# Kernel optimization log

Measured on AMD Instinct MI355X. Metric: run time of the kernel, lower is better.

## Reference

```python
import jax, jax.numpy as jnp
import numpy as np

NEG = -1e30  # finite stand-in for -inf to keep gradients NaN-free


def setup_inputs() -> dict:
    key = jax.random.key(0)
    k1, k2, k3 = jax.random.split(key, 3)
    T, B, V, L = 1600, 48, 1000, 128
    # acoustic model output: already log-softmax normalized, layout [T, B, V]
    logits = jax.random.normal(k1, (T, B, V), dtype=jnp.float32)
    log_probs = jax.nn.log_softmax(logits, axis=-1)
    # flat concatenated targets (nonzero labels; 0 is blank), uniform length L per utt
    targets = jax.random.randint(k2, (B * L,), 1, V, dtype=jnp.int32)
    input_lengths = jax.random.randint(k3, (B,), 3 * T // 4, T + 1, dtype=jnp.int32)
    target_lengths = jnp.full((B,), L, dtype=jnp.int32)
    return {
        "log_probs": log_probs,
        "targets": targets,
        "input_lengths": input_lengths,
        "target_lengths": target_lengths,
    }


def _ctc_neg_log_likelihood(log_probs, targets, input_lengths, target_lengths):
    """Exact log-semiring CTC forward (total score over all alignments),
    equivalent to k2.intersect_dense(ctc_topo o linear_fsa, dense) +
    get_tot_scores(log_semiring=True). Returns -sum_b log p(y_b | x_b).
    log_probs: [T, B, V]; targets: flat [B*L]; lengths: [B].
    """
    T, B, V = log_probs.shape
    L = targets.shape[0] // B
    tg = targets.reshape(B, L)
    S = 2 * L + 1  # blank-interleaved extended label sequence

    ext = jnp.zeros((B, S), dtype=jnp.int32).at[:, 1::2].set(tg)  # [B, S]
    # skip transition s-2 -> s allowed iff label[s] != blank and != label[s-2]
    allow_skip = jnp.concatenate(
        [jnp.zeros((B, 2), dtype=bool),
         (ext[:, 2:] != 0) & (ext[:, 2:] != ext[:, :-2])],
        axis=1,
    )

    def emit(lp_t):  # [B, V] -> [B, S]
        return jnp.take_along_axis(lp_t, ext, axis=1)

    e0 = emit(log_probs[0])
    alpha0 = jnp.full((B, S), NEG, dtype=log_probs.dtype)
    alpha0 = alpha0.at[:, 0].set(e0[:, 0]).at[:, 1].set(e0[:, 1])

    def step(alpha, xs):
        lp_t, t = xs
        prev1 = jnp.pad(alpha[:, :-1], ((0, 0), (1, 0)), constant_values=NEG)
        prev2 = jnp.pad(alpha[:, :-2], ((0, 0), (2, 0)), constant_values=NEG)
        a = jnp.logaddexp(alpha, prev1)
        a = jnp.where(allow_skip, jnp.logaddexp(a, prev2), a)
        new = a + emit(lp_t)
        # freeze alpha once past each utterance's input length
        alpha = jnp.where((t < input_lengths)[:, None], new, alpha)
        return alpha, None

    alpha, _ = jax.lax.scan(step, alpha0, (log_probs[1:], jnp.arange(1, T)))

    # all target_lengths are L, so the final states are S-1 (last blank) and S-2
    tot_scores = jnp.logaddexp(alpha[:, S - 1], alpha[:, S - 2])  # [B]
    return -jnp.sum(tot_scores)


def reference(log_probs, targets, input_lengths, target_lengths):
    return _ctc_neg_log_likelihood(log_probs, targets, input_lengths, target_lengths)
```

## Files before the change

kernel.cpp:

```cpp
#include <hip/hip_runtime.h>
#include <math.h>

#define TT 1600
#define BB 48
#define VV 1000
#define LL 128
#define EMS 132
#define EMTOT (TT*EMS)
#define TILE 60
#define TILEF (TILE*EMS)
#define NTILES ((TT + TILE - 1)/TILE)

__global__ __launch_bounds__(256) void ctc_gather_kernel(
    const float* __restrict__ lp,
    const int* __restrict__ targets,
    float* __restrict__ em)
{
  __shared__ float rowbuf[4][1024];
  const int wv   = threadIdx.x >> 6;
  const int lane = threadIdx.x & 63;
  const int wid  = blockIdx.x * 4 + wv;
  const int t    = wid / BB;
  const int b    = wid - t * BB;

  const float* __restrict__ row = lp + (size_t)wid * VV;
  float* rb = rowbuf[wv];
#pragma unroll
  for (int i = 0; i < 4; i++) {
    int idx = lane + 64 * i;
    if (idx < 250) ((float4*)rb)[idx] = ((const float4*)row)[idx];
  }
  __syncthreads();

  const int* __restrict__ tg = targets + b * LL;
  float* __restrict__ erow = em + (size_t)b * EMTOT + (size_t)t * EMS;
#pragma unroll
  for (int ii = 0; ii < 3; ii++) {
    int k = lane + 64 * ii;
    if (k < 129) {
      int lab = (k == 0) ? 0 : tg[k - 1];
      int pos = (k == 0) ? 0 : (k + 1);
      erow[pos] = __expf(rb[lab]);
    }
  }
}

__global__ __launch_bounds__(128) void ctc_dp_kernel(
    const float* __restrict__ em,
    const int* __restrict__ targets,
    const int* __restrict__ input_lengths,
    float* __restrict__ out)
{
  __shared__ float sbuf[2][TILEF];
  const int b    = blockIdx.x;
  const int lane = threadIdx.x & 63;
  const int wv   = threadIdx.x >> 6;
  const int NS   = input_lengths[b] - 1;
  const float* __restrict__ base = em + (size_t)b * EMTOT;

  float skip1 = 0.f, skip3 = 0.f, m63 = 0.f;
  if (wv == 0) {
    const int* __restrict__ tg = targets + b * LL;
    const int c0  = tg[2 * lane];
    const int c1  = tg[2 * lane + 1];
    const int cm1 = (lane > 0) ? tg[2 * lane - 1] : c0;
    skip1 = (lane > 0 && c0 != cm1) ? 1.0f : 0.0f;
    skip3 = (c1 != c0) ? 1.0f : 0.0f;
    m63   = (lane == 63) ? 1.0f : 0.0f;
  }

  float a0 = 0.f, a1 = 0.f, a2 = 0.f, a3 = 0.f, a4 = 0.f;
  int esum = 0;
  float  pb_r[4];
  float2 ev_r[4];

  if (wv == 1) {
    const float4* src = (const float4*)base;
    float4* dst = (float4*)sbuf[0];
    for (int j = 0; j < 31; j++) {
      int idx = j * 64 + lane;
      if (idx < (TILEF >> 2)) dst[idx] = src[idx];
    }
  }
  __syncthreads();

#define STEP(PB, EV) do {                                            \
    float am1 = __shfl_up(a3, 1);                                    \
    am1 = (lane == 0) ? 0.f : am1;                                   \
    float s0 = a0 + am1;                                             \
    float s1 = fmaf(skip1, am1, a0 + a1);                            \
    float s2 = a1 + a2;                                              \
    float s3 = fmaf(skip3, a1, a2 + a3);                             \
    float s4 = fmaf(a3, m63, a4);                                    \
    a0 = s0 * (PB); a1 = s1 * (EV).x; a2 = s2 * (PB);                \
    a3 = s3 * (EV).y; a4 = s4 * (PB);                                \
  } while (0)

#define RESCALE() do {                                               \
    float mx = fmaxf(fmaxf(fmaxf(a0, a1), fmaxf(a2, a3)), a4);       \
    mx = fmaxf(mx, __shfl_xor(mx, 32));                              \
    mx = fmaxf(mx, __shfl_xor(mx, 16));                              \
    mx = fmaxf(mx, __shfl_xor(mx, 8));                               \
    mx = fmaxf(mx, __shfl_xor(mx, 4));                               \
    mx = fmaxf(mx, __shfl_xor(mx, 2));                               \
    mx = fmaxf(mx, __shfl_xor(mx, 1));                               \
    int eb = (int)((__float_as_uint(mx) >> 23) & 0xFF);              \
    int se = 157 - eb;                       \
    se = se < -126 ? -126 : (se > 127 ? 127 : se);                   \
    float sc = __uint_as_float((unsigned)(se + 127) << 23);          \
    a0 *= sc; a1 *= sc; a2 *= sc; a3 *= sc; a4 *= sc;                \
    esum -= se;                                                      \
  } while (0)

  for (int k = 0; k < NTILES; k++) {
    if (wv == 1) {
      int kn = k + 1;
      if (kn < NTILES) {
        const float4* src = (const float4*)(base + (size_t)kn * TILEF);
        float4* dst = (float4*)sbuf[kn & 1];
        int f4cnt = (EMTOT - kn * TILEF);
        f4cnt = (f4cnt > TILEF ? TILEF : f4cnt) >> 2;
        for (int j = 0; j < 31; j++) {
          int idx = j * 64 + lane;
          if (idx < f4cnt) dst[idx] = src[idx];
        }
      }
    } else {
      const float* lb = sbuf[k & 1];
      if (k == 0 && lane == 0) { a0 = lb[0]; a1 = lb[2]; }
      int tbeg = (k == 0) ? 1 : k * TILE;
      int tend = k * TILE + TILE - 1;
      if (tend > NS) tend = NS;
      int n = tend - tbeg + 1;
      if (n > 0) {
        const int loc0 = tbeg - k * TILE;
        const float* lb0 = lb + loc0 * EMS;
        const float* lbe = lb0 + 2 + 2 * lane;
#define LOADSLOT(D, TF) do {                                         \
    int off_ = (TF) * EMS;                                           \
    pb_r[D] = lb0[off_];                                             \
    ev_r[D] = *(const float2*)(lbe + off_);                          \
  } while (0)
#pragma unroll
        for (int d = 0; d < 4; d++) { if (d < n) LOADSLOT(d, d); }
        int i = 0;
        while (i + 4 <= n) {
#pragma unroll
          for (int d = 0; d < 4; d++) {
            STEP(pb_r[d], ev_r[d]);
            int tf = i + 4 + d;
            if (tf < n) LOADSLOT(d, tf);
          }
          RESCALE();
          i += 4;
        }
#pragma unroll
        for (int d = 0; d < 3; d++) {
          if (i + d < n) STEP(pb_r[d], ev_r[d]);
        }
        if (i < n) RESCALE();
#undef LOADSLOT
      }
    }
    __syncthreads();
  }

  if (wv == 0 && lane == 63) {
    float tot = __logf(a3 + a4) + (float)esum * 0.69314718055994530942f;
    atomicAdd(out, -tot);
  }
#undef STEP
#undef RESCALE
}

extern "C" void kernel_launch(void* const* d_in, const int* in_sizes, int n_in,
                              void* d_out, int out_size, void* d_ws, size_t ws_size,
                              hipStream_t stream) {
  const float* lp            = (const float*)d_in[0];
  const int*   targets       = (const int*)d_in[1];
  const int*   input_lengths = (const int*)d_in[2];

  float* em  = (float*)d_ws;
  float* out = (float*)d_out;

  hipMemsetAsync(out, 0, sizeof(float), stream);

  const int blocks = (TT * BB) / 4;
  ctc_gather_kernel<<<blocks, 256, 0, stream>>>(lp, targets, em);
  ctc_dp_kernel<<<BB, 128, 0, stream>>>(em, targets, input_lengths, out);
}
```

Before: 652.9 us.

## Gather emissions directly, use DPP shuffles and async global-to-LDS tile staging

The gather kernel no longer stages full 1000-wide rows in shared memory. Each wave now reads only the needed label columns for four timesteps straight from global memory, cutting read traffic to the scattered target entries. The DP kernel swaps ds_bpermute-based shuffles for DPP row shifts and broadcasts in the recurrence and max reduction. It also fills LDS tiles with global_load_lds instead of register round-trips. The DPP emulation of the cross-row shift-up depends on lane-select masks and row_bcast semantics, which adds correctness risk on this architecture.

```diff
diff --git a/kernel.cpp b/kernel.cpp
--- a/kernel.cpp
+++ b/kernel.cpp
@@ -9,39 +9,43 @@
 #define EMTOT (TT*EMS)
 #define TILE 60
 #define TILEF (TILE*EMS)
-#define NTILES ((TT + TILE - 1)/TILE)
+#define NTILES 27
+
+#define DPPF(x, ctrl) __int_as_float(__builtin_amdgcn_update_dpp( \
+    0, __float_as_int(x), (ctrl), 0xf, 0xf, true))
 
 __global__ __launch_bounds__(256) void ctc_gather_kernel(
     const float* __restrict__ lp,
     const int* __restrict__ targets,
     float* __restrict__ em)
 {
-  __shared__ float rowbuf[4][1024];
   const int wv   = threadIdx.x >> 6;
   const int lane = threadIdx.x & 63;
-  const int wid  = blockIdx.x * 4 + wv;
-  const int t    = wid / BB;
-  const int b    = wid - t * BB;
-
-  const float* __restrict__ row = lp + (size_t)wid * VV;
-  float* rb = rowbuf[wv];
-#pragma unroll
-  for (int i = 0; i < 4; i++) {
-    int idx = lane + 64 * i;
-    if (idx < 250) ((float4*)rb)[idx] = ((const float4*)row)[idx];
-  }
-  __syncthreads();
+  const int gw   = blockIdx.x * 4 + wv;
+  const int b    = gw % BB;
+  const int t0   = (gw / BB) * 4;
 
   const int* __restrict__ tg = targets + b * LL;
-  float* __restrict__ erow = em + (size_t)b * EMTOT + (size_t)t * EMS;
+  const int g0 = (lane == 0) ? 0 : tg[lane - 1];
+  const int g1 = tg[lane + 63];
+  const int g2 = tg[127];
+  const int p0 = (lane == 0) ? 0 : (lane + 1);
+  const int p1 = lane + 65;
+
+  float v0[4], v1[4], v2[4];
 #pragma unroll
-  for (int ii = 0; ii < 3; ii++) {
-    int k = lane + 64 * ii;
-    if (k < 129) {
-      int lab = (k == 0) ? 0 : tg[k - 1];
-      int pos = (k == 0) ? 0 : (k + 1);
-      erow[pos] = __expf(rb[lab]);
-    }
+  for (int r = 0; r < 4; r++) {
+    const float* row = lp + ((size_t)(t0 + r) * BB + b) * VV;
+    v0[r] = row[g0];
+    v1[r] = row[g1];
+    if (lane == 0) v2[r] = row[g2];
+  }
+#pragma unroll
+  for (int r = 0; r < 4; r++) {
+    float* erow = em + (size_t)b * EMTOT + (size_t)(t0 + r) * EMS;
+    erow[p0] = __expf(v0[r]);
+    erow[p1] = __expf(v1[r]);
+    if (lane == 0) erow[129] = __expf(v2[r]);
   }
 }
 
@@ -58,15 +62,17 @@
   const int NS   = input_lengths[b] - 1;
   const float* __restrict__ base = em + (size_t)b * EMTOT;
 
-  float skip1 = 0.f, skip3 = 0.f, m63 = 0.f;
+  float skip1 = 0.f, skip3 = 0.f, m63 = 0.f, sel1648 = 0.f, sel32 = 0.f;
   if (wv == 0) {
     const int* __restrict__ tg = targets + b * LL;
     const int c0  = tg[2 * lane];
     const int c1  = tg[2 * lane + 1];
     const int cm1 = (lane > 0) ? tg[2 * lane - 1] : c0;
-    skip1 = (lane > 0 && c0 != cm1) ? 1.0f : 0.0f;
-    skip3 = (c1 != c0) ? 1.0f : 0.0f;
-    m63   = (lane == 63) ? 1.0f : 0.0f;
+    skip1   = (lane > 0 && c0 != cm1) ? 1.0f : 0.0f;
+    skip3   = (c1 != c0) ? 1.0f : 0.0f;
+    m63     = (lane == 63) ? 1.0f : 0.0f;
+    sel1648 = (lane == 16 || lane == 48) ? 1.0f : 0.0f;
+    sel32   = (lane == 32) ? 1.0f : 0.0f;
   }
 
   float a0 = 0.f, a1 = 0.f, a2 = 0.f, a3 = 0.f, a4 = 0.f;
@@ -74,19 +80,27 @@
   float  pb_r[4];
   float2 ev_r[4];
 
-  if (wv == 1) {
-    const float4* src = (const float4*)base;
-    float4* dst = (float4*)sbuf[0];
-    for (int j = 0; j < 31; j++) {
-      int idx = j * 64 + lane;
-      if (idx < (TILEF >> 2)) dst[idx] = src[idx];
-    }
-  }
-  __syncthreads();
+#define STAGE(KN) do {                                               \
+    const float4* src_ = (const float4*)(base + (size_t)(KN) * TILEF); \
+    float* dst_ = sbuf[(KN) & 1];                                    \
+    const int nf4_ = ((KN) == NTILES - 1) ? 1320 : 1980;             \
+    _Pragma("unroll")                                                \
+    for (int j = 0; j < 31; j++) {                                   \
+      int idx_ = (j << 6) + lane;                                    \
+      if (idx_ < nf4_)                                               \
+        __builtin_amdgcn_global_load_lds(                            \
+            (const __attribute__((address_space(1))) unsigned int*)(src_ + idx_), \
+            (__attribute__((address_space(3))) unsigned int*)(dst_ + (j << 8)),   \
+            16, 0, 0);                                               \
+    }                                                                \
+  } while (0)
 
 #define STEP(PB, EV) do {                                            \
-    float am1 = __shfl_up(a3, 1);                                    \
-    am1 = (lane == 0) ? 0.f : am1;                                   \
+    float am1 = DPPF(a3, 0x111);                     \
+    float h15 = DPPF(a3, 0x142);                    \
+    float h31 = DPPF(a3, 0x143);                    \
+    am1 = fmaf(sel1648, h15, am1);                                   \
+    am1 = fmaf(sel32,   h31, am1);                                   \
     float s0 = a0 + am1;                                             \
     float s1 = fmaf(skip1, am1, a0 + a1);                            \
     float s2 = a1 + a2;                                              \
@@ -98,13 +112,13 @@
 
 #define RESCALE() do {                                               \
     float mx = fmaxf(fmaxf(fmaxf(a0, a1), fmaxf(a2, a3)), a4);       \
-    mx = fmaxf(mx, __shfl_xor(mx, 32));                              \
-    mx = fmaxf(mx, __shfl_xor(mx, 16));                              \
-    mx = fmaxf(mx, __shfl_xor(mx, 8));                               \
-    mx = fmaxf(mx, __shfl_xor(mx, 4));                               \
-    mx = fmaxf(mx, __shfl_xor(mx, 2));                               \
-    mx = fmaxf(mx, __shfl_xor(mx, 1));                               \
-    int eb = (int)((__float_as_uint(mx) >> 23) & 0xFF);              \
+    mx = fmaxf(mx, DPPF(mx, 0x111));                  \
+    mx = fmaxf(mx, DPPF(mx, 0x112));                  \
+    mx = fmaxf(mx, DPPF(mx, 0x114));                  \
+    mx = fmaxf(mx, DPPF(mx, 0x118));                  \
+    mx = fmaxf(mx, DPPF(mx, 0x142));                    \
+    mx = fmaxf(mx, DPPF(mx, 0x143));      \
+    int eb = (__builtin_amdgcn_readlane(__float_as_int(mx), 63) >> 23) & 0xFF; \
     int se = 157 - eb;                       \
     se = se < -126 ? -126 : (se > 127 ? 127 : se);                   \
     float sc = __uint_as_float((unsigned)(se + 127) << 23);          \
@@ -112,19 +126,12 @@
     esum -= se;                                                      \
   } while (0)
 
+  if (wv == 1) STAGE(0);
+  __syncthreads();
+
   for (int k = 0; k < NTILES; k++) {
     if (wv == 1) {
-      int kn = k + 1;
-      if (kn < NTILES) {
-        const float4* src = (const float4*)(base + (size_t)kn * TILEF);
-        float4* dst = (float4*)sbuf[kn & 1];
-        int f4cnt = (EMTOT - kn * TILEF);
-        f4cnt = (f4cnt > TILEF ? TILEF : f4cnt) >> 2;
-        for (int j = 0; j < 31; j++) {
-          int idx = j * 64 + lane;
-          if (idx < f4cnt) dst[idx] = src[idx];
-        }
-      }
+      if (k + 1 < NTILES) STAGE(k + 1);
     } else {
       const float* lb = sbuf[k & 1];
       if (k == 0 && lane == 0) { a0 = lb[0]; a1 = lb[2]; }
@@ -133,8 +140,7 @@
       if (tend > NS) tend = NS;
       int n = tend - tbeg + 1;
       if (n > 0) {
-        const int loc0 = tbeg - k * TILE;
-        const float* lb0 = lb + loc0 * EMS;
+        const float* lb0 = lb + (tbeg - k * TILE) * EMS;
         const float* lbe = lb0 + 2 + 2 * lane;
 #define LOADSLOT(D, TF) do {                                         \
     int off_ = (TF) * EMS;                                           \
@@ -171,6 +177,7 @@
   }
 #undef STEP
 #undef RESCALE
+#undef STAGE
 }
 
 extern "C" void kernel_launch(void* const* d_in, const int* in_sizes, int n_in,
@@ -185,7 +192,6 @@
 
   hipMemsetAsync(out, 0, sizeof(float), stream);
 
-  const int blocks = (TT * BB) / 4;
-  ctc_gather_kernel<<<blocks, 256, 0, stream>>>(lp, targets, em);
+  ctc_gather_kernel<<<4800, 256, 0, stream>>>(lp, targets, em);
   ctc_dp_kernel<<<BB, 128, 0, stream>>>(em, targets, input_lengths, out);
 }
```

Result: faster. 563.3 us (-13.7%).
